# Kernel tuning notes

Measured on AMD Instinct MI355X. Metric: run time of the kernel, lower is better.

Reference implementation:

```python
import jax, jax.numpy as jnp
import numpy as np

N = 100000   # nodes per type
E = 500000   # edges per edge type
HID = 128    # hidden_channels
H = 4        # heads
D = HID // H # head dim = 32
L = 2        # layers
T = 2        # node types: 0=user, 1=item
R = 2        # edge types: 0=user->item, 1=item->user


def setup_inputs() -> dict:
    key = jax.random.key(0)
    ks = jax.random.split(key, 16)
    s = jnp.float32(0.05)
    f32 = jnp.float32
    return {
        "x_user": jax.random.normal(ks[0], (N, HID), f32),
        "x_item": jax.random.normal(ks[1], (N, HID), f32),
        "W_in": jax.random.normal(ks[2], (T, HID, HID), f32) * s,
        "b_in": jnp.zeros((T, HID), f32),
        "Wk": jax.random.normal(ks[3], (L, T, HID, HID), f32) * s,
        "bk": jnp.zeros((L, T, HID), f32),
        "Wq": jax.random.normal(ks[4], (L, T, HID, HID), f32) * s,
        "bq": jnp.zeros((L, T, HID), f32),
        "Wv": jax.random.normal(ks[5], (L, T, HID, HID), f32) * s,
        "bv": jnp.zeros((L, T, HID), f32),
        "a_rel": jax.random.normal(ks[6], (L, R, H, D, D), f32) * s,
        "m_rel": jax.random.normal(ks[7], (L, R, H, D, D), f32) * s,
        "p_rel": jnp.ones((L, R, H), f32),
        "Wo": jax.random.normal(ks[8], (L, T, HID, HID), f32) * s,
        "bo": jnp.zeros((L, T, HID), f32),
        "skip": jnp.zeros((L, T), f32),
        "edge_ui": jax.random.randint(ks[9], (2, E), 0, N, dtype=jnp.int32),
        "edge_iu": jax.random.randint(ks[10], (2, E), 0, N, dtype=jnp.int32),
    }


def _seg_softmax(logits, seg, n):
    # numerically stable softmax over edges grouped by destination node
    m = jax.ops.segment_max(logits, seg, num_segments=n)            # [N,H]
    m = jnp.where(jnp.isfinite(m), m, jnp.float32(0.0))
    e = jnp.exp(logits - m[seg])                                    # [E,H]
    z = jax.ops.segment_sum(e, seg, num_segments=n)                 # [N,H]
    return e / (z[seg] + jnp.float32(1e-16))


def reference(x_user, x_item, W_in, b_in, Wk, bk, Wq, bq, Wv, bv,
              a_rel, m_rel, p_rel, Wo, bo, skip, edge_ui, edge_iu):
    scale = jnp.float32(1.0 / np.sqrt(D))
    # per-node-type input linear + relu (lin_dict)
    h = [jax.nn.relu(x_user @ W_in[0] + b_in[0]),
         jax.nn.relu(x_item @ W_in[1] + b_in[1])]
    # (edge_type_id, src_type, dst_type, edge_index)
    etypes = [(0, 0, 1, edge_ui), (1, 1, 0, edge_iu)]
    for l in range(L):
        k = [(h[t] @ Wk[l, t] + bk[l, t]).reshape(N, H, D) for t in range(T)]
        q = [(h[t] @ Wq[l, t] + bq[l, t]).reshape(N, H, D) for t in range(T)]
        v = [(h[t] @ Wv[l, t] + bv[l, t]).reshape(N, H, D) for t in range(T)]
        agg = [jnp.zeros((N, H, D), h[0].dtype) for _ in range(T)]
        for r, st, dt, e in etypes:
            src, dst = e[0], e[1]
            # relation-specific transforms applied on node table (N < E)
            k_r = jnp.einsum('nhd,hde->nhe', k[st], a_rel[l, r])
            v_r = jnp.einsum('nhd,hde->nhe', v[st], m_rel[l, r])
            logits = jnp.sum(q[dt][dst] * k_r[src], axis=-1) * p_rel[l, r] * scale  # [E,H]
            alpha = _seg_softmax(logits, dst, N)                                    # [E,H]
            msg = alpha[:, :, None] * v_r[src]                                      # [E,H,D]
            agg[dt] = agg[dt] + jax.ops.segment_sum(msg, dst, num_segments=N)
        h_new = []
        for t in range(T):
            out = agg[t].reshape(N, HID)
            a = jax.nn.gelu(out, approximate=False) @ Wo[l, t] + bo[l, t]
            beta = jax.nn.sigmoid(skip[l, t])
            hn = beta * a + (1.0 - beta) * h[t]
            if l > 0:  # model-level residual (i > 0 in torch code)
                hn = hn + h[t]
            h_new.append(hn)
        h = h_new
    return jnp.stack(h)  # [T, N, HID]
```

## Files before the change

### kernel.cpp

```cpp
#include <hip/hip_runtime.h>
#include <stdint.h>
#include <stdio.h>

#define NN 100000
#define NE 500000
#define HID 128
#define NH 4
#define HD 32
#define LL 2
#define SCANB 1024
#define NB ((NN + SCANB - 1) / SCANB)

typedef unsigned short u16;
typedef unsigned char u8;
typedef unsigned int u32;
typedef __attribute__((ext_vector_type(8))) short bfrag;
typedef __attribute__((ext_vector_type(4))) float f32x4;
typedef __attribute__((ext_vector_type(2))) float f32x2;

__device__ __forceinline__ float b2f(u32 lo16) {
  union { u32 u; float f; } c; c.u = lo16; return c.f;
}
__device__ __forceinline__ u16 f2b(float f) {
  union { float f; u32 u; } c; c.f = f;
  u32 u = c.u;
  u32 r = (u + 0x7FFFu + ((u >> 16) & 1u)) >> 16;
  return (u16)r;
}
__device__ __forceinline__ float geluf(float x) {
  return 0.5f * x * (1.0f + erff(x * 0.70710678118654752f));
}
__device__ __forceinline__ void up8(uint4 a, float* f) {
  f[0] = b2f(a.x << 16); f[1] = b2f(a.x & 0xFFFF0000u);
  f[2] = b2f(a.y << 16); f[3] = b2f(a.y & 0xFFFF0000u);
  f[4] = b2f(a.z << 16); f[5] = b2f(a.z & 0xFFFF0000u);
  f[6] = b2f(a.w << 16); f[7] = b2f(a.w & 0xFFFF0000u);
}

__global__ __launch_bounds__(256) void csr_count(const int* __restrict__ edges,
                                                 int* __restrict__ deg) {
  int e = blockIdx.x * blockDim.x + threadIdx.x;
  if (e < NE) atomicAdd(&deg[edges[NE + e]], 1);
}

__global__ __launch_bounds__(SCANB) void scan1(const int* __restrict__ deg,
                                               int* __restrict__ rowptr,
                                               int* __restrict__ bsum) {
  __shared__ int ls[SCANB];
  int t = threadIdx.x;
  int g = blockIdx.x * SCANB + t;
  int v = (g < NN) ? deg[g] : 0;
  ls[t] = v;
  __syncthreads();
#pragma unroll
  for (int off = 1; off < SCANB; off <<= 1) {
    int u = (t >= off) ? ls[t - off] : 0;
    __syncthreads();
    ls[t] += u;
    __syncthreads();
  }
  if (g < NN) rowptr[g] = ls[t] - v;
  if (t == SCANB - 1) bsum[blockIdx.x] = ls[t];
}

__global__ __launch_bounds__(128) void scan2(int* __restrict__ bsum,
                                             int* __restrict__ boff) {
  __shared__ int ls[128];
  int t = threadIdx.x;
  int v = (t < NB) ? bsum[t] : 0;
  ls[t] = v;
  __syncthreads();
#pragma unroll
  for (int off = 1; off < 128; off <<= 1) {
    int u = (t >= off) ? ls[t - off] : 0;
    __syncthreads();
    ls[t] += u;
    __syncthreads();
  }
  if (t < NB) boff[t] = ls[t] - v;
}

__global__ __launch_bounds__(SCANB) void scan3(int* __restrict__ rowptr,
                                               int* __restrict__ cursor,
                                               const int* __restrict__ boff) {
  int g = blockIdx.x * SCANB + threadIdx.x;
  if (g < NN) {
    int v = rowptr[g] + boff[blockIdx.x];
    rowptr[g] = v;
    cursor[g] = v;
  }
  if (g == 0) rowptr[NN] = NE;
}

__global__ __launch_bounds__(256) void csr_fill(const int* __restrict__ edges,
                                                int* __restrict__ cursor,
                                                int* __restrict__ srcs) {
  int e = blockIdx.x * blockDim.x + threadIdx.x;
  if (e < NE) {
    int pos = atomicAdd(&cursor[edges[NE + e]], 1);
    srcs[pos] = edges[e];
  }
}

__global__ __launch_bounds__(256) void hist_deg(const int* __restrict__ rowptr,
                                                int* __restrict__ hist) {
  __shared__ int lh[64];
  if (threadIdx.x < 64) lh[threadIdx.x] = 0;
  __syncthreads();
  int d = blockIdx.x * 256 + threadIdx.x;
  if (d < NN) {
    int dg = rowptr[d + 1] - rowptr[d];
    atomicAdd(&lh[dg < 63 ? dg : 63], 1);
  }
  __syncthreads();
  if (threadIdx.x < 64 && lh[threadIdx.x])
    atomicAdd(&hist[threadIdx.x], lh[threadIdx.x]);
}

__global__ __launch_bounds__(64) void scan_hist(const int* __restrict__ hist,
                                                int* __restrict__ hcur) {
  __shared__ int ls[64];
  int t = threadIdx.x;
  int v = hist[t];
  ls[t] = v;
  __syncthreads();
#pragma unroll
  for (int off = 1; off < 64; off <<= 1) {
    int u = (t >= off) ? ls[t - off] : 0;
    __syncthreads();
    ls[t] += u;
    __syncthreads();
  }
  hcur[t] = ls[t] - v;
}

__global__ __launch_bounds__(256) void scatter_deg(const int* __restrict__ rowptr,
                                                   int* __restrict__ hcur,
                                                   int* __restrict__ order) {
  __shared__ int lh[64];
  __shared__ int lbase[64];
  if (threadIdx.x < 64) lh[threadIdx.x] = 0;
  __syncthreads();
  int d = blockIdx.x * 256 + threadIdx.x;
  int dg = 0, rank = 0;
  if (d < NN) {
    dg = rowptr[d + 1] - rowptr[d];
    if (dg > 63) dg = 63;
    rank = atomicAdd(&lh[dg], 1);
  }
  __syncthreads();
  if (threadIdx.x < 64)
    lbase[threadIdx.x] = lh[threadIdx.x] ? atomicAdd(&hcur[threadIdx.x], lh[threadIdx.x]) : 0;
  __syncthreads();
  if (d < NN) order[lbase[dg] + rank] = d;
}

__global__ __launch_bounds__(256) void prep_wT(const float* __restrict__ src, size_t srcStride,
                                               u16* __restrict__ dst, size_t dstStride,
                                               const float* __restrict__ bsrc, int bsStride,
                                               float* __restrict__ bdst, int bdStride,
                                               const float* __restrict__ p_rel_q) {
  int m = blockIdx.y;
  const float* S = src + (size_t)m * srcStride;
  u16* D = dst + (size_t)m * dstStride;
  int idx = blockIdx.x * 256 + threadIdx.x;
  int k = idx >> 7, n = idx & 127;
  float v = S[idx];
  if (p_rel_q != nullptr) {
    int l = m >> 1, t = m & 1;
    v *= p_rel_q[((l << 1) | (1 - t)) * NH + (n >> 5)] * 0.17677669529663687f;
  }
  D[(size_t)n * HID + k] = f2b(v);
  if (bsrc != nullptr && blockIdx.x == 0 && threadIdx.x < HID) {
    int col = threadIdx.x;
    float bvv = bsrc[(size_t)m * bsStride + col];
    if (p_rel_q != nullptr) {
      int l = m >> 1, t = m & 1;
      bvv *= p_rel_q[((l << 1) | (1 - t)) * NH + (col >> 5)] * 0.17677669529663687f;
    }
    bdst[(size_t)m * bdStride + col] = bvv;
  }
}

__global__ __launch_bounds__(256) void combine_all(
    const float* __restrict__ Wk, const float* __restrict__ bk,
    const float* __restrict__ Wv, const float* __restrict__ bv,
    const float* __restrict__ a_rel, const float* __restrict__ m_rel,
    u16* __restrict__ wqkvT, float* __restrict__ bqkv) {
  int l = blockIdx.z;
  int t = blockIdx.y >> 1, which = blockIdx.y & 1;
  const float* W  = (which == 0 ? Wk : Wv) + (size_t)(l * 2 + t) * HID * HID;
  const float* b  = (which == 0 ? bk : bv) + (size_t)(l * 2 + t) * HID;
  const float* Ar = (which == 0 ? a_rel : m_rel) + (size_t)(l * 2 + t) * NH * HD * HD;
  u16* Wd = wqkvT + ((size_t)(l * 2 + t) * 3 + 1 + which) * HID * HID;
  float* bd = bqkv + ((size_t)(l * 2 + t) * 3 + 1 + which) * HID;
  int idx = blockIdx.x * 256 + threadIdx.x;
  int i = idx >> 7, col = idx & 127;
  int h = col >> 5, e = col & 31;
  {
    const float* ap = Ar + h * HD * HD + e;
    const float* wp = W + (size_t)i * HID + h * HD;
    float s = 0.f;
#pragma unroll
    for (int d = 0; d < HD; ++d) s += wp[d] * ap[d * HD];
    Wd[(size_t)col * HID + i] = f2b(s);
  }
  if (blockIdx.x == 0 && threadIdx.x < HID) {
    int col2 = threadIdx.x, h2 = col2 >> 5, e2 = col2 & 31;
    const float* ap = Ar + h2 * HD * HD + e2;
    const float* bp = b + h2 * HD;
    float s = 0.f;
#pragma unroll
    for (int d = 0; d < HD; ++d) s += bp[d] * ap[d * HD];
    bd[col2] = s;
  }
}

template <int NMAT, bool RELU, bool SKIP, bool FP8KV, bool AF32>
__global__ __launch_bounds__(256) void mfgemm(
    const void* __restrict__ A0, const void* __restrict__ A1, int M, int gb,
    const u16* __restrict__ WT, size_t wtStride,
    const float* __restrict__ bias, size_t biasStride,
    u16* __restrict__ O00, u16* __restrict__ O01, u16* __restrict__ O02,
    u16* __restrict__ O10, u16* __restrict__ O11, u16* __restrict__ O12,
    float* __restrict__ Of0, float* __restrict__ Of1,
    const u16* __restrict__ hp0, const u16* __restrict__ hp1,
    const float* __restrict__ skipP, int resflag) {
  __shared__ __align__(16) u16 sW[HID * HID];
  const int t = blockIdx.x >= gb;
  const int bx = t ? blockIdx.x - gb : blockIdx.x;
  const void* A = t ? A1 : A0;
  const u16* Wg = WT + (size_t)t * wtStride;
  const float* bs = bias + (size_t)t * biasStride;
  u16* Os[3];
  Os[0] = t ? O10 : O00; Os[1] = t ? O11 : O01; Os[2] = t ? O12 : O02;
  float* Of = t ? Of1 : Of0;
  const u16* hprev = t ? hp1 : hp0;

  const int lane = threadIdx.x & 63;
  const int wid = threadIdx.x >> 6;
  const int l16 = lane & 15, g = lane >> 4;
  const int rbase = bx * 128 + wid * 32;

  float beta = 0.f;
  if (SKIP) beta = 1.f / (1.f + __expf(-skipP[t]));

  auto stageW = [&](int m) {
    const u16* Wm = Wg + (size_t)m * HID * HID;
#pragma unroll
    for (int j = 0; j < 8; ++j) {
      int ins = wid * 8 + j;
      int o16 = ins * 64 + lane;
      int row = o16 >> 4, ch = o16 & 15;
      const u16* src = Wm + (size_t)row * HID + ((ch ^ (row & 7)) << 3);
      u16* dst = sW + (size_t)ins * 512;
      __builtin_amdgcn_global_load_lds(
          (const __attribute__((address_space(1))) unsigned int*)src,
          (__attribute__((address_space(3))) unsigned int*)dst, 16, 0, 0);
    }
  };

  bfrag af[2][4];
  int rowA[2];
#pragma unroll
  for (int rt = 0; rt < 2; ++rt) {
    int row = rbase + rt * 16 + l16;
    rowA[rt] = row;
    int rl = row < M ? row : M - 1;
    if (AF32) {
      const float* apf = (const float*)A + (size_t)rl * HID;
#pragma unroll
      for (int ks = 0; ks < 4; ++ks) {
        float4 u0 = *(const float4*)(apf + (ks * 4 + g) * 8);
        float4 u1 = *(const float4*)(apf + (ks * 4 + g) * 8 + 4);
        union { u16 s[8]; bfrag b; } pk;
        pk.s[0] = f2b(u0.x); pk.s[1] = f2b(u0.y); pk.s[2] = f2b(u0.z); pk.s[3] = f2b(u0.w);
        pk.s[4] = f2b(u1.x); pk.s[5] = f2b(u1.y); pk.s[6] = f2b(u1.z); pk.s[7] = f2b(u1.w);
        af[rt][ks] = pk.b;
      }
    } else {
      const bfrag* ap = (const bfrag*)A + (size_t)rl * (HID / 8);
#pragma unroll
      for (int ks = 0; ks < 4; ++ks) af[rt][ks] = ap[ks * 4 + g];
    }
  }

  stageW(0);
  __syncthreads();

#pragma unroll
  for (int m = 0; m < NMAT; ++m) {
    f32x4 acc[2][8];
#pragma unroll
    for (int rt = 0; rt < 2; ++rt)
#pragma unroll
      for (int ct = 0; ct < 8; ++ct) acc[rt][ct] = (f32x4){0.f, 0.f, 0.f, 0.f};
#pragma unroll
    for (int ct = 0; ct < 8; ++ct) {
      int row = ct * 16 + l16;
      bfrag wf[4];
#pragma unroll
      for (int ks = 0; ks < 4; ++ks)
        wf[ks] = *(const bfrag*)&sW[(size_t)row * HID + (((ks * 4 + g) ^ (row & 7)) << 3)];
#pragma unroll
      for (int ks = 0; ks < 4; ++ks)
#pragma unroll
        for (int rt = 0; rt < 2; ++rt)
          acc[rt][ct] = __builtin_amdgcn_mfma_f32_16x16x32_bf16(wf[ks], af[rt][ks],
                                                                acc[rt][ct], 0, 0, 0);
    }
    if (m + 1 < NMAT) {
      __syncthreads();
      stageW(m + 1);
    }
    u16* Ob = Os[m];
#pragma unroll
    for (int rt = 0; rt < 2; ++rt) {
      int row = rowA[rt];
      if (row >= M) continue;
#pragma unroll
      for (int ct = 0; ct < 8; ++ct) {
        int nc = ct * 16 + g * 4;
        const float4 bb = *(const float4*)(bs + m * HID + nc);
        float o0 = acc[rt][ct][0] + bb.x;
        float o1 = acc[rt][ct][1] + bb.y;
        float o2 = acc[rt][ct][2] + bb.z;
        float o3 = acc[rt][ct][3] + bb.w;
        if (RELU) {
          o0 = fmaxf(o0, 0.f); o1 = fmaxf(o1, 0.f);
          o2 = fmaxf(o2, 0.f); o3 = fmaxf(o3, 0.f);
        }
        if (SKIP) {
          uint2 hh2 = *(const uint2*)(hprev + (size_t)row * HID + nc);
          float h0 = b2f(hh2.x << 16), h1 = b2f(hh2.x & 0xFFFF0000u);
          float h2 = b2f(hh2.y << 16), h3 = b2f(hh2.y & 0xFFFF0000u);
          o0 = beta * o0 + (1.f - beta) * h0;
          o1 = beta * o1 + (1.f - beta) * h1;
          o2 = beta * o2 + (1.f - beta) * h2;
          o3 = beta * o3 + (1.f - beta) * h3;
          if (resflag) { o0 += h0; o1 += h1; o2 += h2; o3 += h3; }
        }
        if (FP8KV && m >= 1) {
          u32 pk = __builtin_amdgcn_cvt_pk_fp8_f32(o0, o1, 0u, false);
          pk = __builtin_amdgcn_cvt_pk_fp8_f32(o2, o3, pk, true);
          *(u32*)((u8*)Ob + (size_t)row * HID + nc) = pk;
        } else {
          if (Ob != nullptr) {
            u32 lo = (u32)f2b(o0) | ((u32)f2b(o1) << 16);
            u32 hi = (u32)f2b(o2) | ((u32)f2b(o3) << 16);
            *(uint2*)(Ob + (size_t)row * HID + nc) = make_uint2(lo, hi);
          }
          if (NMAT == 1 && Of != nullptr) {
            *(float4*)(Of + (size_t)row * HID + nc) = make_float4(o0, o1, o2, o3);
          }
        }
      }
    }
    if (m + 1 < NMAT) __syncthreads();
  }
}

__global__ __launch_bounds__(256) void agg_csr(
    const int* __restrict__ rp0, const int* __restrict__ ss0, const int* __restrict__ od0,
    const u16* __restrict__ q0, const u8* __restrict__ k0,
    const u8* __restrict__ v0, u16* __restrict__ o0,
    const int* __restrict__ rp1, const int* __restrict__ ss1, const int* __restrict__ od1,
    const u16* __restrict__ q1, const u8* __restrict__ k1,
    const u8* __restrict__ v1, u16* __restrict__ o1, int agb) {
  const int r = blockIdx.x >= agb;
  const int bx = r ? blockIdx.x - agb : blockIdx.x;
  int i = bx * 256 + threadIdx.x;
  if (i >= NN * NH) return;
  const int* rowptr = r ? rp1 : rp0;
  const int* srcs = r ? ss1 : ss0;
  const int* order = r ? od1 : od0;
  const u16* qT = r ? q1 : q0;
  const u8* kT = r ? k1 : k0;
  const u8* vT = r ? v1 : v0;
  u16* aggb = r ? o1 : o0;

  int dst = order[i >> 2], h = i & 3;
  float qv[HD];
  {
    const uint4* qp = (const uint4*)(qT + (size_t)dst * HID + h * HD);
#pragma unroll
    for (int j = 0; j < 4; ++j) up8(qp[j], qv + j * 8);
  }
  float acc[HD];
#pragma unroll
  for (int j = 0; j < HD; ++j) acc[j] = 0.f;
  float z = 0.f;
  int b = rowptr[dst], e2 = rowptr[dst + 1];
  for (int idx = b; idx < e2; ++idx) {
    int src = srcs[idx];
    const uint4* kp = (const uint4*)(kT + (size_t)src * HID + h * HD);
    const uint4* vp = (const uint4*)(vT + (size_t)src * HID + h * HD);
    uint4 ka0 = kp[0], ka1 = kp[1];
    uint4 va0 = vp[0], va1 = vp[1];
    u32 kw[8] = {ka0.x, ka0.y, ka0.z, ka0.w, ka1.x, ka1.y, ka1.z, ka1.w};
    u32 vw[8] = {va0.x, va0.y, va0.z, va0.w, va1.x, va1.y, va1.z, va1.w};
    float s = 0.f;
#pragma unroll
    for (int j = 0; j < 8; ++j) {
      f32x2 p0 = __builtin_amdgcn_cvt_pk_f32_fp8(kw[j], false);
      f32x2 p1 = __builtin_amdgcn_cvt_pk_f32_fp8(kw[j], true);
      s += qv[4 * j] * p0.x + qv[4 * j + 1] * p0.y + qv[4 * j + 2] * p1.x + qv[4 * j + 3] * p1.y;
    }
    s = fminf(s, 60.f);
    float ev = __expf(s);
    z += ev;
#pragma unroll
    for (int j = 0; j < 8; ++j) {
      f32x2 p0 = __builtin_amdgcn_cvt_pk_f32_fp8(vw[j], false);
      f32x2 p1 = __builtin_amdgcn_cvt_pk_f32_fp8(vw[j], true);
      acc[4 * j] += ev * p0.x; acc[4 * j + 1] += ev * p0.y;
      acc[4 * j + 2] += ev * p1.x; acc[4 * j + 3] += ev * p1.y;
    }
  }
  float inv = 1.f / (z + 1e-16f);
  u16* ap = aggb + (size_t)dst * HID + h * HD;
  u32 w[16];
#pragma unroll
  for (int j = 0; j < 16; ++j) {
    float a0 = geluf(acc[2 * j] * inv);
    float a1 = geluf(acc[2 * j + 1] * inv);
    w[j] = (u32)f2b(a0) | ((u32)f2b(a1) << 16);
  }
#pragma unroll
  for (int j = 0; j < 4; ++j)
    *(uint4*)(ap + j * 8) = make_uint4(w[4 * j], w[4 * j + 1], w[4 * j + 2], w[4 * j + 3]);
}

extern "C" void kernel_launch(void* const* d_in, const int* in_sizes, int n_in,
                              void* d_out, int out_size, void* d_ws, size_t ws_size,
                              hipStream_t stream) {
  const float* x_user = (const float*)d_in[0];
  const float* x_item = (const float*)d_in[1];
  const float* W_in = (const float*)d_in[2];
  const float* b_in = (const float*)d_in[3];
  const float* Wk = (const float*)d_in[4];
  const float* bk = (const float*)d_in[5];
  const float* Wq = (const float*)d_in[6];
  const float* bq = (const float*)d_in[7];
  const float* Wv = (const float*)d_in[8];
  const float* bv = (const float*)d_in[9];
  const float* a_rel = (const float*)d_in[10];
  const float* m_rel = (const float*)d_in[11];
  const float* p_rel = (const float*)d_in[12];
  const float* Wo = (const float*)d_in[13];
  const float* bo = (const float*)d_in[14];
  const float* skipP = (const float*)d_in[15];
  const int* edge_ui = (const int*)d_in[16];
  const int* edge_iu = (const int*)d_in[17];
  float* out = (float*)d_out;

  char* p = (char*)d_ws;
  auto take = [&](size_t bytes) {
    void* r = (void*)p;
    p += (bytes + 255) & ~(size_t)255;
    return r;
  };
  size_t nodeB = (size_t)NN * HID * sizeof(u16);
  size_t node8 = (size_t)NN * HID;
  u16* hb[2] = {(u16*)take(nodeB), (u16*)take(nodeB)};
  u16* qb[2] = {(u16*)take(nodeB), (u16*)take(nodeB)};
  u8* kb[2] = {(u8*)take(node8), (u8*)take(node8)};
  u8* vb[2] = {(u8*)take(node8), (u8*)take(node8)};
  u16* aggb[2] = {(u16*)take(nodeB), (u16*)take(nodeB)};
  int* deg    = (int*)take((size_t)NN * 4);
  int* cursor = (int*)take((size_t)NN * 4);
  int* bsum   = (int*)take((size_t)NB * 4);
  int* boff   = (int*)take((size_t)NB * 4);
  int* hist   = (int*)take((size_t)64 * 4);
  int* hcur   = (int*)take((size_t)64 * 4);
  int* rowptr[2] = {(int*)take((size_t)(NN + 1) * 4), (int*)take((size_t)(NN + 1) * 4)};
  int* srcs[2]   = {(int*)take((size_t)NE * 4), (int*)take((size_t)NE * 4)};
  int* order[2]  = {(int*)take((size_t)NN * 4), (int*)take((size_t)NN * 4)};
  u16* winT  = (u16*)take((size_t)2 * HID * HID * 2);
  u16* woT   = (u16*)take((size_t)4 * HID * HID * 2);
  u16* wqkvT = (u16*)take((size_t)2 * 2 * 3 * HID * HID * 2);
  float* bqkv = (float*)take((size_t)2 * 2 * 3 * HID * 4);
  size_t used = (size_t)(p - (char*)d_ws);
  if (used > ws_size) {
    fprintf(stderr, "HGT kernel: workspace too small: need %zu, have %zu\n", used, ws_size);
    return;
  }

  const int GB = (NN + 127) / 128;
  const int EB = (NE + 255) / 256;
  const int DB = (NN + 255) / 256;
  dim3 blk(256);
  const int* eidx[2] = {edge_ui, edge_iu};

  for (int r = 0; r < 2; ++r) {
    hipMemsetAsync(deg, 0, (size_t)NN * 4, stream);
    csr_count<<<EB, blk, 0, stream>>>(eidx[r], deg);
    scan1<<<NB, SCANB, 0, stream>>>(deg, rowptr[r], bsum);
    scan2<<<1, 128, 0, stream>>>(bsum, boff);
    scan3<<<NB, SCANB, 0, stream>>>(rowptr[r], cursor, boff);
    csr_fill<<<EB, blk, 0, stream>>>(eidx[r], cursor, srcs[r]);
    hipMemsetAsync(hist, 0, 64 * 4, stream);
    hist_deg<<<DB, blk, 0, stream>>>(rowptr[r], hist);
    scan_hist<<<1, 64, 0, stream>>>(hist, hcur);
    scatter_deg<<<DB, blk, 0, stream>>>(rowptr[r], hcur, order[r]);
  }

  prep_wT<<<dim3(64, 2), blk, 0, stream>>>(W_in, HID * HID, winT, HID * HID,
                                           nullptr, 0, nullptr, 0, nullptr);
  prep_wT<<<dim3(64, 4), blk, 0, stream>>>(Wo, HID * HID, woT, HID * HID,
                                           nullptr, 0, nullptr, 0, nullptr);
  prep_wT<<<dim3(64, 4), blk, 0, stream>>>(Wq, HID * HID, wqkvT, 3 * HID * HID,
                                           bq, HID, bqkv, 3 * HID, p_rel);
  combine_all<<<dim3(64, 4, 2), blk, 0, stream>>>(Wk, bk, Wv, bv, a_rel, m_rel,
                                                  wqkvT, bqkv);

  mfgemm<1, true, false, false, true><<<2 * GB, blk, 0, stream>>>(
      x_user, x_item, NN, GB, winT, HID * HID, b_in, HID,
      hb[0], nullptr, nullptr, hb[1], nullptr, nullptr,
      nullptr, nullptr, nullptr, nullptr, nullptr, 0);

  const int AGB = (NN * NH + 255) / 256;
  for (int l = 0; l < LL; ++l) {
    mfgemm<3, false, false, true, false><<<2 * GB, blk, 0, stream>>>(
        hb[0], hb[1], NN, GB,
        wqkvT + (size_t)l * 2 * 3 * HID * HID, 3 * HID * HID,
        bqkv + (size_t)l * 2 * 3 * HID, 3 * HID,
        qb[0], (u16*)kb[0], (u16*)vb[0], qb[1], (u16*)kb[1], (u16*)vb[1],
        nullptr, nullptr, nullptr, nullptr, nullptr, 0);
    agg_csr<<<2 * AGB, blk, 0, stream>>>(
        rowptr[0], srcs[0], order[0], qb[1], kb[0], vb[0], aggb[1],
        rowptr[1], srcs[1], order[1], qb[0], kb[1], vb[1], aggb[0], AGB);
    if (l == 0) {
      mfgemm<1, false, true, false, false><<<2 * GB, blk, 0, stream>>>(
          aggb[0], aggb[1], NN, GB,
          woT, HID * HID, bo, HID,
          hb[0], nullptr, nullptr, hb[1], nullptr, nullptr,
          nullptr, nullptr, hb[0], hb[1], skipP, 0);
    } else {
      mfgemm<1, false, true, false, false><<<2 * GB, blk, 0, stream>>>(
          aggb[0], aggb[1], NN, GB,
          woT + (size_t)2 * HID * HID, HID * HID, bo + 2 * HID, HID,
          nullptr, nullptr, nullptr, nullptr, nullptr, nullptr,
          out, out + (size_t)NN * HID, hb[0], hb[1], skipP + 2, 1);
    }
  }
}
```

Measured before the change: 557.4 us.

## Batch CSR build across edge types and split QKV GEMM into persistent per-matrix blocks

```diff
diff --git a/kernel.cpp b/kernel.cpp
--- a/kernel.cpp
+++ b/kernel.cpp
@@ -10,6 +10,7 @@
 #define LL 2
 #define SCANB 1024
 #define NB ((NN + SCANB - 1) / SCANB)
+#define QCH 130
 
 typedef unsigned short u16;
 typedef unsigned char u8;
@@ -37,19 +38,23 @@
   f[6] = b2f(a.w << 16); f[7] = b2f(a.w & 0xFFFF0000u);
 }
 
-__global__ __launch_bounds__(256) void csr_count(const int* __restrict__ edges,
+__global__ __launch_bounds__(256) void csr_count(const int* __restrict__ e0,
+                                                 const int* __restrict__ e1,
                                                  int* __restrict__ deg) {
-  int e = blockIdx.x * blockDim.x + threadIdx.x;
-  if (e < NE) atomicAdd(&deg[edges[NE + e]], 1);
+  int r = blockIdx.y;
+  const int* edges = r ? e1 : e0;
+  int e = blockIdx.x * 256 + threadIdx.x;
+  if (e < NE) atomicAdd(&deg[(size_t)r * NN + edges[NE + e]], 1);
 }
 
 __global__ __launch_bounds__(SCANB) void scan1(const int* __restrict__ deg,
-                                               int* __restrict__ rowptr,
+                                               int* __restrict__ rp,
                                                int* __restrict__ bsum) {
   __shared__ int ls[SCANB];
+  int r = blockIdx.y;
   int t = threadIdx.x;
   int g = blockIdx.x * SCANB + t;
-  int v = (g < NN) ? deg[g] : 0;
+  int v = (g < NN) ? deg[(size_t)r * NN + g] : 0;
   ls[t] = v;
   __syncthreads();
 #pragma unroll
@@ -59,15 +64,16 @@
     ls[t] += u;
     __syncthreads();
   }
-  if (g < NN) rowptr[g] = ls[t] - v;
-  if (t == SCANB - 1) bsum[blockIdx.x] = ls[t];
-}
-
-__global__ __launch_bounds__(128) void scan2(int* __restrict__ bsum,
+  if (g < NN) rp[(size_t)r * (NN + 1) + g] = ls[t] - v;
+  if (t == SCANB - 1) bsum[r * NB + blockIdx.x] = ls[t];
+}
+
+__global__ __launch_bounds__(128) void scan2(const int* __restrict__ bsum,
                                              int* __restrict__ boff) {
   __shared__ int ls[128];
+  int r = blockIdx.y;
   int t = threadIdx.x;
-  int v = (t < NB) ? bsum[t] : 0;
+  int v = (t < NB) ? bsum[r * NB + t] : 0;
   ls[t] = v;
   __syncthreads();
 #pragma unroll
@@ -77,51 +83,60 @@
     ls[t] += u;
     __syncthreads();
   }
-  if (t < NB) boff[t] = ls[t] - v;
-}
-
-__global__ __launch_bounds__(SCANB) void scan3(int* __restrict__ rowptr,
+  if (t < NB) boff[r * NB + t] = ls[t] - v;
+}
+
+__global__ __launch_bounds__(SCANB) void scan3(int* __restrict__ rp,
                                                int* __restrict__ cursor,
                                                const int* __restrict__ boff) {
+  int r = blockIdx.y;
   int g = blockIdx.x * SCANB + threadIdx.x;
   if (g < NN) {
-    int v = rowptr[g] + boff[blockIdx.x];
-    rowptr[g] = v;
-    cursor[g] = v;
-  }
-  if (g == 0) rowptr[NN] = NE;
-}
-
-__global__ __launch_bounds__(256) void csr_fill(const int* __restrict__ edges,
+    int v = rp[(size_t)r * (NN + 1) + g] + boff[r * NB + blockIdx.x];
+    rp[(size_t)r * (NN + 1) + g] = v;
+    cursor[(size_t)r * NN + g] = v;
+  }
+  if (g == 0) rp[(size_t)r * (NN + 1) + NN] = NE;
+}
+
+__global__ __launch_bounds__(256) void csr_fill(const int* __restrict__ e0,
+                                                const int* __restrict__ e1,
                                                 int* __restrict__ cursor,
-                                                int* __restrict__ srcs) {
-  int e = blockIdx.x * blockDim.x + threadIdx.x;
+                                                int* __restrict__ s0,
+                                                int* __restrict__ s1) {
+  int r = blockIdx.y;
+  const int* edges = r ? e1 : e0;
+  int* srcs = r ? s1 : s0;
+  int e = blockIdx.x * 256 + threadIdx.x;
   if (e < NE) {
-    int pos = atomicAdd(&cursor[edges[NE + e]], 1);
+    int pos = atomicAdd(&cursor[(size_t)r * NN + edges[NE + e]], 1);
     srcs[pos] = edges[e];
   }
 }
 
-__global__ __launch_bounds__(256) void hist_deg(const int* __restrict__ rowptr,
+__global__ __launch_bounds__(256) void hist_deg(const int* __restrict__ rp,
                                                 int* __restrict__ hist) {
   __shared__ int lh[64];
+  int r = blockIdx.y;
   if (threadIdx.x < 64) lh[threadIdx.x] = 0;
   __syncthreads();
   int d = blockIdx.x * 256 + threadIdx.x;
   if (d < NN) {
+    const int* rowptr = rp + (size_t)r * (NN + 1);
     int dg = rowptr[d + 1] - rowptr[d];
     atomicAdd(&lh[dg < 63 ? dg : 63], 1);
   }
   __syncthreads();
   if (threadIdx.x < 64 && lh[threadIdx.x])
-    atomicAdd(&hist[threadIdx.x], lh[threadIdx.x]);
+    atomicAdd(&hist[r * 64 + threadIdx.x], lh[threadIdx.x]);
 }
 
 __global__ __launch_bounds__(64) void scan_hist(const int* __restrict__ hist,
                                                 int* __restrict__ hcur) {
   __shared__ int ls[64];
+  int r = blockIdx.y;
   int t = threadIdx.x;
-  int v = hist[t];
+  int v = hist[r * 64 + t];
   ls[t] = v;
   __syncthreads();
 #pragma unroll
@@ -131,26 +146,30 @@
     ls[t] += u;
     __syncthreads();
   }
-  hcur[t] = ls[t] - v;
-}
-
-__global__ __launch_bounds__(256) void scatter_deg(const int* __restrict__ rowptr,
+  hcur[r * 64 + t] = ls[t] - v;
+}
+
+__global__ __launch_bounds__(256) void scatter_deg(const int* __restrict__ rp,
                                                    int* __restrict__ hcur,
-                                                   int* __restrict__ order) {
+                                                   int* __restrict__ o0,
+                                                   int* __restrict__ o1) {
   __shared__ int lh[64];
   __shared__ int lbase[64];
+  int r = blockIdx.y;
+  int* order = r ? o1 : o0;
   if (threadIdx.x < 64) lh[threadIdx.x] = 0;
   __syncthreads();
   int d = blockIdx.x * 256 + threadIdx.x;
   int dg = 0, rank = 0;
   if (d < NN) {
+    const int* rowptr = rp + (size_t)r * (NN + 1);
     dg = rowptr[d + 1] - rowptr[d];
     if (dg > 63) dg = 63;
     rank = atomicAdd(&lh[dg], 1);
   }
   __syncthreads();
   if (threadIdx.x < 64)
-    lbase[threadIdx.x] = lh[threadIdx.x] ? atomicAdd(&hcur[threadIdx.x], lh[threadIdx.x]) : 0;
+    lbase[threadIdx.x] = lh[threadIdx.x] ? atomicAdd(&hcur[r * 64 + threadIdx.x], lh[threadIdx.x]) : 0;
   __syncthreads();
   if (d < NN) order[lbase[dg] + rank] = d;
 }
@@ -213,6 +232,98 @@
 #pragma unroll
     for (int d = 0; d < HD; ++d) s += bp[d] * ap[d * HD];
     bd[col2] = s;
+  }
+}
+
+__global__ __launch_bounds__(256) void qkv_gemm(
+    const u16* __restrict__ h0, const u16* __restrict__ h1,
+    const u16* __restrict__ WT,
+    const float* __restrict__ bias,
+    u16* __restrict__ q0, u16* __restrict__ q1,
+    u8* __restrict__ k0, u8* __restrict__ k1,
+    u8* __restrict__ v0, u8* __restrict__ v1) {
+  __shared__ __align__(16) u16 sW[HID * HID];
+  const int z = blockIdx.y;
+  const int t = z >= 3 ? 1 : 0;
+  const int mat = z - t * 3;
+  const u16* A = t ? h1 : h0;
+  const u16* Wm = WT + ((size_t)t * 3 + mat) * HID * HID;
+  const float* bs = bias + ((size_t)t * 3 + mat) * HID;
+  u16* Oq = t ? q1 : q0;
+  u8* O8 = (mat == 1) ? (t ? k1 : k0) : (t ? v1 : v0);
+
+  const int lane = threadIdx.x & 63;
+  const int wid = threadIdx.x >> 6;
+  const int l16 = lane & 15, g = lane >> 4;
+
+#pragma unroll
+  for (int j = 0; j < 8; ++j) {
+    int ins = wid * 8 + j;
+    int o16 = ins * 64 + lane;
+    int row = o16 >> 4, ch = o16 & 15;
+    const u16* src = Wm + (size_t)row * HID + ((ch ^ (row & 7)) << 3);
+    u16* dst = sW + (size_t)ins * 512;
+    __builtin_amdgcn_global_load_lds(
+        (const __attribute__((address_space(1))) unsigned int*)src,
+        (__attribute__((address_space(3))) unsigned int*)dst, 16, 0, 0);
+  }
+  __syncthreads();
+
+  for (int c = blockIdx.x; c * 128 < NN; c += gridDim.x) {
+    const int rbase = c * 128 + wid * 32;
+    bfrag af[2][4];
+    int rowA[2];
+#pragma unroll
+    for (int rt = 0; rt < 2; ++rt) {
+      int row = rbase + rt * 16 + l16;
+      rowA[rt] = row;
+      int rl = row < NN ? row : NN - 1;
+      const bfrag* ap = (const bfrag*)(A + (size_t)rl * HID);
+#pragma unroll
+      for (int ks = 0; ks < 4; ++ks) af[rt][ks] = ap[ks * 4 + g];
+    }
+    f32x4 acc[2][8];
+#pragma unroll
+    for (int rt = 0; rt < 2; ++rt)
+#pragma unroll
+      for (int ct = 0; ct < 8; ++ct) acc[rt][ct] = (f32x4){0.f, 0.f, 0.f, 0.f};
+#pragma unroll
+    for (int ct = 0; ct < 8; ++ct) {
+      int row = ct * 16 + l16;
+      bfrag wf[4];
+#pragma unroll
+      for (int ks = 0; ks < 4; ++ks)
+        wf[ks] = *(const bfrag*)&sW[(size_t)row * HID + (((ks * 4 + g) ^ (row & 7)) << 3)];
+#pragma unroll
+      for (int ks = 0; ks < 4; ++ks)
+#pragma unroll
+        for (int rt = 0; rt < 2; ++rt)
+          acc[rt][ct] = __builtin_amdgcn_mfma_f32_16x16x32_bf16(wf[ks], af[rt][ks],
+                                                                acc[rt][ct], 0, 0, 0);
+    }
+#pragma unroll
+    for (int rt = 0; rt < 2; ++rt) {
+      int row = rowA[rt];
+      if (row >= NN) continue;
+#pragma unroll
+      for (int ct = 0; ct < 8; ++ct) {
+        int nc = ct * 16 + g * 4;
+        const float4 bb = *(const float4*)(bs + nc);
+        float o0 = acc[rt][ct][0] + bb.x;
+        float o1 = acc[rt][ct][1] + bb.y;
+        float o2 = acc[rt][ct][2] + bb.z;
+        float o3 = acc[rt][ct][3] + bb.w;
+        if (mat == 0) {
+          u32 lo = (u32)f2b(o0) | ((u32)f2b(o1) << 16);
+          u32 hi = (u32)f2b(o2) | ((u32)f2b(o3) << 16);
+          *(uint2*)(Oq + (size_t)row * HID + nc) = make_uint2(lo, hi);
+        } else {
+          u32 pk = __builtin_amdgcn_cvt_pk_fp8_f32(o0, o1, 0u, false);
+          pk = __builtin_amdgcn_cvt_pk_fp8_f32(o2, o3, pk, true);
+          *(u32*)(O8 + (size_t)row * HID + nc) = pk;
+        }
+      }
+    }
   }
 }
 
@@ -467,15 +578,15 @@
   u8* kb[2] = {(u8*)take(node8), (u8*)take(node8)};
   u8* vb[2] = {(u8*)take(node8), (u8*)take(node8)};
   u16* aggb[2] = {(u16*)take(nodeB), (u16*)take(nodeB)};
-  int* deg    = (int*)take((size_t)NN * 4);
-  int* cursor = (int*)take((size_t)NN * 4);
-  int* bsum   = (int*)take((size_t)NB * 4);
-  int* boff   = (int*)take((size_t)NB * 4);
-  int* hist   = (int*)take((size_t)64 * 4);
-  int* hcur   = (int*)take((size_t)64 * 4);
-  int* rowptr[2] = {(int*)take((size_t)(NN + 1) * 4), (int*)take((size_t)(NN + 1) * 4)};
-  int* srcs[2]   = {(int*)take((size_t)NE * 4), (int*)take((size_t)NE * 4)};
-  int* order[2]  = {(int*)take((size_t)NN * 4), (int*)take((size_t)NN * 4)};
+  int* deg2   = (int*)take((size_t)2 * NN * 4);
+  int* cur2   = (int*)take((size_t)2 * NN * 4);
+  int* bsum2  = (int*)take((size_t)2 * NB * 4);
+  int* boff2  = (int*)take((size_t)2 * NB * 4);
+  int* hist2  = (int*)take((size_t)2 * 64 * 4);
+  int* hcur2  = (int*)take((size_t)2 * 64 * 4);
+  int* rp2    = (int*)take((size_t)2 * (NN + 1) * 4);
+  int* srcs[2]  = {(int*)take((size_t)NE * 4), (int*)take((size_t)NE * 4)};
+  int* order[2] = {(int*)take((size_t)NN * 4), (int*)take((size_t)NN * 4)};
   u16* winT  = (u16*)take((size_t)2 * HID * HID * 2);
   u16* woT   = (u16*)take((size_t)4 * HID * HID * 2);
   u16* wqkvT = (u16*)take((size_t)2 * 2 * 3 * HID * HID * 2);
@@ -490,20 +601,18 @@
   const int EB = (NE + 255) / 256;
   const int DB = (NN + 255) / 256;
   dim3 blk(256);
-  const int* eidx[2] = {edge_ui, edge_iu};
-
-  for (int r = 0; r < 2; ++r) {
-    hipMemsetAsync(deg, 0, (size_t)NN * 4, stream);
-    csr_count<<<EB, blk, 0, stream>>>(eidx[r], deg);
-    scan1<<<NB, SCANB, 0, stream>>>(deg, rowptr[r], bsum);
-    scan2<<<1, 128, 0, stream>>>(bsum, boff);
-    scan3<<<NB, SCANB, 0, stream>>>(rowptr[r], cursor, boff);
-    csr_fill<<<EB, blk, 0, stream>>>(eidx[r], cursor, srcs[r]);
-    hipMemsetAsync(hist, 0, 64 * 4, stream);
-    hist_deg<<<DB, blk, 0, stream>>>(rowptr[r], hist);
-    scan_hist<<<1, 64, 0, stream>>>(hist, hcur);
-    scatter_deg<<<DB, blk, 0, stream>>>(rowptr[r], hcur, order[r]);
-  }
+
+  hipMemsetAsync(deg2, 0, (size_t)2 * NN * 4, stream);
+  csr_count<<<dim3(EB, 2), blk, 0, stream>>>(edge_ui, edge_iu, deg2);
+  scan1<<<dim3(NB, 2), SCANB, 0, stream>>>(deg2, rp2, bsum2);
+  scan2<<<dim3(1, 2), 128, 0, stream>>>(bsum2, boff2);
+  scan3<<<dim3(NB, 2), SCANB, 0, stream>>>(rp2, cur2, boff2);
+  csr_fill<<<dim3(EB, 2), blk, 0, stream>>>(edge_ui, edge_iu, cur2, srcs[0], srcs[1]);
+  hipMemsetAsync(hist2, 0, 2 * 64 * 4, stream);
+  hist_deg<<<dim3(DB, 2), blk, 0, stream>>>(rp2, hist2);
+  scan_hist<<<dim3(1, 2), 64, 0, stream>>>(hist2, hcur2);
+  scatter_deg<<<dim3(DB, 2), blk, 0, stream>>>(rp2, hcur2, order[0], order[1]);
+  int* rowptr[2] = {rp2, rp2 + (NN + 1)};
 
   prep_wT<<<dim3(64, 2), blk, 0, stream>>>(W_in, HID * HID, winT, HID * HID,
                                            nullptr, 0, nullptr, 0, nullptr);
@@ -521,12 +630,11 @@
 
   const int AGB = (NN * NH + 255) / 256;
   for (int l = 0; l < LL; ++l) {
-    mfgemm<3, false, false, true, false><<<2 * GB, blk, 0, stream>>>(
-        hb[0], hb[1], NN, GB,
-        wqkvT + (size_t)l * 2 * 3 * HID * HID, 3 * HID * HID,
-        bqkv + (size_t)l * 2 * 3 * HID, 3 * HID,
-        qb[0], (u16*)kb[0], (u16*)vb[0], qb[1], (u16*)kb[1], (u16*)vb[1],
-        nullptr, nullptr, nullptr, nullptr, nullptr, 0);
+    qkv_gemm<<<dim3(QCH, 6), blk, 0, stream>>>(
+        hb[0], hb[1],
+        wqkvT + (size_t)l * 2 * 3 * HID * HID,
+        bqkv + (size_t)l * 2 * 3 * HID,
+        qb[0], qb[1], kb[0], kb[1], vb[0], vb[1]);
     agg_csr<<<2 * AGB, blk, 0, stream>>>(
         rowptr[0], srcs[0], order[0], qb[1], kb[0], vb[0], aggb[1],
         rowptr[1], srcs[1], order[1], qb[0], kb[1], vb[1], aggb[0], AGB);
```

Result: slower. 634.6 us (+13.8%).
